# Kernel tuning notes

Measured on AMD Instinct MI355X. Metric: run time of the kernel, lower is better.

Reference implementation:

```python
import jax, jax.numpy as jnp
import numpy as np

NHEAD = 8
DILATED = 1


def setup_inputs() -> dict:
    key = jax.random.key(0)
    ks = jax.random.split(key, 5)
    bs, c, h, w, k = 2, 256, 128, 128, 8
    L = (h // 2) * (w // 2)
    return {
        "query": jax.random.normal(ks[0], (bs, c, h, w), jnp.float32),
        "key": jax.random.normal(ks[1], (bs, c, h, w), jnp.float32),
        "value": jax.random.normal(ks[2], (bs, c, h, w), jnp.float32),
        "topk_pos": jax.random.randint(ks[3], (bs, L, k, 2), 0, h // 2, dtype=jnp.int32).astype(jnp.int64),
        "rel_pos": jax.random.normal(ks[4], (bs, NHEAD, h, w, 4 * k), jnp.float32),
    }


def reference(query, key, value, topk_pos, rel_pos):
    bs, c, h0, w0 = query.shape
    h1, w1 = key.shape[2], key.shape[3]
    nh = NHEAD
    d = c // nh
    L = (h0 // 2) * (w0 // 2)
    k = topk_pos.shape[2]
    k4 = 4 * k

    # key/value: [b,c,h,w] -> [b, h1*w1, nh, d]
    kf = key.reshape(bs, c, h1 * w1).transpose(0, 2, 1).reshape(bs, h1 * w1, nh, d)
    vf = value.reshape(bs, c, h1 * w1).transpose(0, 2, 1).reshape(bs, h1 * w1, nh, d)

    # query grouped into 2x2 blocks: [b, L, 4, nh, d]
    q = query.reshape(bs, nh, d, h0 // 2, 2, w0 // 2, 2)
    q = q.transpose(0, 3, 5, 4, 6, 1, 2).reshape(bs, L, 4, nh, d)

    # build gather indices into flattened key grid (offsets by dilation)
    tp = topk_pos * 2                               # [b, L, k, 2]
    row, col = tp[..., 0], tp[..., 1]
    offs = [(0, 0), (0, DILATED), (DILATED, 0), (DILATED, DILATED)]
    idx = jnp.stack([(row + x) * w1 + (col + y) for x, y in offs], axis=3)  # [b,L,k,4]
    idx = jnp.clip(idx, 0, h1 * w1 - 1).reshape(bs, L, k4)

    def gather(tbl):  # tbl: [b, h1*w1, nh, d] -> [b, L, k4, nh, d]
        return jax.vmap(lambda t, i: t[i])(tbl, idx.reshape(bs, L * k4)).reshape(bs, L, k4, nh, d)

    kg = gather(kf)
    vg = gather(vf)

    scale = 1.0 / np.sqrt(d).astype(np.float32)
    qk = jnp.einsum('blthd,blmhd->bltmh', q, kg) * scale  # [b,L,4,k4,nh]

    rp = rel_pos.reshape(bs, nh, h0 // 2, 2, w0 // 2, 2, k4)
    rp = rp.transpose(0, 2, 4, 3, 5, 6, 1).reshape(bs, L, 4, k4, nh)
    qk = qk + rp

    A = jax.nn.softmax(qk, axis=-2)  # softmax over the k*4 candidate axis
    msg = jnp.einsum('bltmh,blmhd->blthd', A, vg)  # [b,L,4,nh,d]

    # un-group 2x2 blocks back to full resolution: [b, h0*w0, c]
    msg = msg.reshape(bs, h0 // 2, w0 // 2, 2, 2, nh, d)
    msg = msg.transpose(0, 1, 3, 2, 4, 5, 6).reshape(bs, h0 * w0, c)

    up_idx = jnp.broadcast_to(idx[:, :, None, :], (bs, L, 4, k4))
    up_idx = up_idx.reshape(bs, h0 // 2, w0 // 2, 2, 2, k4)
    up_idx = up_idx.transpose(0, 1, 3, 2, 4, 5).reshape(bs, h0 * w0, k4)
    return msg, up_idx
```

## Files before the change

### kernel.cpp

```cpp
#include <hip/hip_runtime.h>
#include <hip/hip_fp16.h>
#include <math.h>

constexpr int NH = 8;
constexpr int D = 32;
constexpr int C = 256;
constexpr int H0 = 128;
constexpr int W0 = 128;
constexpr int PIX = H0 * W0;
constexpr int LBLK = 4096;
constexpr int K4 = 32;
constexpr int KSTH = 260;
constexpr int KST = 258;

__global__ __launch_bounds__(256) void transpose_qkv_kernel(
    const float* __restrict__ q, const float* __restrict__ k,
    const float* __restrict__ v, float* __restrict__ qT,
    __half* __restrict__ kT, __half* __restrict__ vT)
{
  __shared__ float tile[64 * 65];
  const int z = blockIdx.z;
  const int b = z & 1;
  const int arr = z >> 1;
  const float* src = (arr == 0 ? q : arr == 1 ? k : v) + (size_t)b * C * PIX;

  const int p0 = blockIdx.x * 64;
  const int c0 = blockIdx.y * 64;
  const int t15 = threadIdx.x & 15;
  const int thi4 = threadIdx.x >> 4;

#pragma unroll
  for (int r = 0; r < 4; ++r) {
    const int ch = thi4 + r * 16;
    const int p4 = t15 * 4;
    float4 f = *(const float4*)&src[(size_t)(c0 + ch) * PIX + p0 + p4];
    tile[(p4 + 0) * 65 + ch] = f.x;
    tile[(p4 + 1) * 65 + ch] = f.y;
    tile[(p4 + 2) * 65 + ch] = f.z;
    tile[(p4 + 3) * 65 + ch] = f.w;
  }
  __syncthreads();

  if (arr == 0) {
    float* dst = qT + (size_t)b * PIX * C;
#pragma unroll
    for (int r = 0; r < 4; ++r) {
      const int p = thi4 + r * 16;
      const int c4 = t15 * 4;
      const float* tr = &tile[p * 65 + c4];
      *(float4*)&dst[(size_t)(p0 + p) * C + c0 + c4] =
          make_float4(tr[0], tr[1], tr[2], tr[3]);
    }
  } else {
    __half* dst = (arr == 1 ? kT : vT) + (size_t)b * PIX * C;
    const int t7 = threadIdx.x & 7;
    const int th8 = threadIdx.x >> 3;
#pragma unroll
    for (int r = 0; r < 2; ++r) {
      const int p = th8 + r * 32;
      const int c8 = t7 * 8;
      const float* tr = &tile[p * 65 + c8];
      __half2 h0 = __floats2half2_rn(tr[0], tr[1]);
      __half2 h1 = __floats2half2_rn(tr[2], tr[3]);
      __half2 h2 = __floats2half2_rn(tr[4], tr[5]);
      __half2 h3 = __floats2half2_rn(tr[6], tr[7]);
      uint4 u;
      u.x = *(unsigned*)&h0; u.y = *(unsigned*)&h1;
      u.z = *(unsigned*)&h2; u.w = *(unsigned*)&h3;
      *(uint4*)&dst[(size_t)(p0 + p) * C + c0 + c8] = u;
    }
  }
}

__global__ __launch_bounds__(256) void cascade_attn_f16(
    const float* __restrict__ qT,
    const __half* __restrict__ kT,
    const __half* __restrict__ vT,
    const int* __restrict__ topk,
    const float* __restrict__ relp,
    float* __restrict__ out_msg,
    float* __restrict__ out_idx)
{
  __shared__ __half kvh[K4 * KSTH];
  __shared__ float qa[4 * C];

  const int tid = threadIdx.x;
  const int bid = blockIdx.x;
  const int b = bid >> 12;
  const int l = bid & (LBLK - 1);
  const int by = l >> 6, bx = l & 63;
  const int r0 = by * 2, c0 = bx * 2;

  const int* tp = topk + ((size_t)b * LBLK + l) * 16;

  const int h = tid >> 5;
  const int m = tid & 31;

  {
    const int t = tid >> 6, ln = tid & 63;
    const int pix = r0 * W0 + c0 + (t >> 1) * W0 + (t & 1);
    float4 f = *(const float4*)&qT[((size_t)b * PIX + pix) * C + ln * 4];
    *(float4*)&qa[t * C + ln * 4] = f;
  }

  const int p = tid >> 3;
  const int ln8 = tid & 7;
  const int jj = p >> 2, o = p & 3;
  const int gpix = (tp[jj * 2] * 2 + (o >> 1)) * W0 + tp[jj * 2 + 1] * 2 + (o & 1);

  {
    const __half* src = &kT[((size_t)b * PIX + gpix) * C + ln8 * 8];
#pragma unroll
    for (int i = 0; i < 4; ++i) {
      uint4 f = *(const uint4*)(src + i * 64);
      __half* dst = &kvh[p * KSTH + ln8 * 8 + i * 64];
      *(uint2*)dst = make_uint2(f.x, f.y);
      *(uint2*)(dst + 4) = make_uint2(f.z, f.w);
    }
  }

  uint4 vreg[4];
  {
    const __half* src = &vT[((size_t)b * PIX + gpix) * C + ln8 * 8];
#pragma unroll
    for (int i = 0; i < 4; ++i) vreg[i] = *(const uint4*)(src + i * 64);
  }

  const size_t rb = ((((size_t)b * NH + h) * H0 + r0) * W0 + c0) * K4 + m;
  float rl0 = relp[rb];
  float rl1 = relp[rb + K4];
  float rl2 = relp[rb + (size_t)W0 * K4];
  float rl3 = relp[rb + (size_t)W0 * K4 + K4];

  if (tid < 128) {
    const int mm = tid & 31, t = tid >> 5;
    const int j2 = mm >> 2, o2 = mm & 3;
    const int pix = (tp[j2 * 2] * 2 + (o2 >> 1)) * W0 + tp[j2 * 2 + 1] * 2 + (o2 & 1);
    const int prow = r0 + (t >> 1), pcol = c0 + (t & 1);
    out_idx[((size_t)b * PIX + prow * W0 + pcol) * K4 + mm] = (float)pix;
  }
  __syncthreads();

  float a0 = 0.f, a1 = 0.f, a2 = 0.f, a3 = 0.f;
#pragma unroll
  for (int dq = 0; dq < 8; ++dq) {
    const int off = h * D + dq * 4;
    float4 q0 = *(const float4*)&qa[0 * C + off];
    float4 q1 = *(const float4*)&qa[1 * C + off];
    float4 q2 = *(const float4*)&qa[2 * C + off];
    float4 q3 = *(const float4*)&qa[3 * C + off];
    uint2 kraw = *(const uint2*)&kvh[m * KSTH + off];
    __half2 kh0 = *(__half2*)&kraw.x;
    __half2 kh1 = *(__half2*)&kraw.y;
    float2 ka = __half22float2(kh0);
    float2 kc = __half22float2(kh1);
    a0 += q0.x * ka.x + q0.y * ka.y + q0.z * kc.x + q0.w * kc.y;
    a1 += q1.x * ka.x + q1.y * ka.y + q1.z * kc.x + q1.w * kc.y;
    a2 += q2.x * ka.x + q2.y * ka.y + q2.z * kc.x + q2.w * kc.y;
    a3 += q3.x * ka.x + q3.y * ka.y + q3.z * kc.x + q3.w * kc.y;
  }

  const float scale = 0.17677669529663687f;
  float sv[4];
  sv[0] = a0 * scale + rl0;
  sv[1] = a1 * scale + rl1;
  sv[2] = a2 * scale + rl2;
  sv[3] = a3 * scale + rl3;

  float pr4[4];
#pragma unroll
  for (int t = 0; t < 4; ++t) {
    float x = sv[t];
    float mx = x;
#pragma unroll
    for (int off = 16; off > 0; off >>= 1) mx = fmaxf(mx, __shfl_xor(mx, off));
    float pbit = __expf(x - mx);
    float sm = pbit;
#pragma unroll
    for (int off = 16; off > 0; off >>= 1) sm += __shfl_xor(sm, off);
    pr4[t] = pbit / sm;
  }
  __syncthreads();

  *(float4*)&qa[tid * 4] = make_float4(pr4[0], pr4[1], pr4[2], pr4[3]);
#pragma unroll
  for (int i = 0; i < 4; ++i) {
    __half* dst = &kvh[p * KSTH + ln8 * 8 + i * 64];
    *(uint2*)dst = make_uint2(vreg[i].x, vreg[i].y);
    *(uint2*)(dst + 4) = make_uint2(vreg[i].z, vreg[i].w);
  }
  __syncthreads();

  float o0 = 0.f, o1 = 0.f, o2 = 0.f, o3 = 0.f;
#pragma unroll
  for (int mm = 0; mm < 32; ++mm) {
    float4 a4 = *(const float4*)&qa[(h * K4 + mm) * 4];
    float vv = __half2float(kvh[mm * KSTH + h * D + m]);
    o0 += a4.x * vv;
    o1 += a4.y * vv;
    o2 += a4.z * vv;
    o3 += a4.w * vv;
  }
  const size_t ob = ((size_t)b * PIX + (size_t)r0 * W0 + c0) * C + h * D + m;
  out_msg[ob] = o0;
  out_msg[ob + C] = o1;
  out_msg[ob + (size_t)W0 * C] = o2;
  out_msg[ob + (size_t)W0 * C + C] = o3;
}

__global__ __launch_bounds__(256) void cascade_attn_fallback(
    const float* __restrict__ query, const float* __restrict__ key,
    const float* __restrict__ value, const int* __restrict__ topk,
    const float* __restrict__ relp, float* __restrict__ out_msg,
    float* __restrict__ out_idx)
{
  __shared__ float kv[K4 * KST];
  __shared__ float qs[4 * C];
  __shared__ float as_[NH * K4 * 4];

  const int tid = threadIdx.x;
  const int bid = blockIdx.x;
  const int b = bid >> 12;
  const int l = bid & (LBLK - 1);
  const int by = l >> 6, bx = l & 63;
  const int r0 = by * 2, c0 = bx * 2;

  const size_t plane = (size_t)PIX;
  const float* qb = query + (size_t)b * C * plane;
  const float* kb = key + (size_t)b * C * plane;
  const float* vb = value + (size_t)b * C * plane;
  const int* tp = topk + ((size_t)b * LBLK + l) * 16;

  {
    const float* qp = qb + (size_t)tid * plane + r0 * W0 + c0;
    float2 a = *(const float2*)qp;
    float2 bb = *(const float2*)(qp + W0);
    qs[0 * C + tid] = a.x; qs[1 * C + tid] = a.y;
    qs[2 * C + tid] = bb.x; qs[3 * C + tid] = bb.y;
  }
#pragma unroll
  for (int it = 0; it < 16; ++it) {
    const int jj = it >> 1, x = it & 1;
    const int pr = tp[jj * 2] * 2 + x;
    const int pc = tp[jj * 2 + 1] * 2;
    float2 f = *(const float2*)(kb + (size_t)tid * plane + pr * W0 + pc);
    const int m0 = jj * 4 + x * 2;
    kv[m0 * KST + tid] = f.x;
    kv[(m0 + 1) * KST + tid] = f.y;
  }
  if (tid < 128) {
    const int m = tid & 31, t = tid >> 5;
    const int jj = m >> 2, o = m & 3;
    const int pix = (tp[jj * 2] * 2 + (o >> 1)) * W0 + tp[jj * 2 + 1] * 2 + (o & 1);
    const int prow = r0 + (t >> 1), pcol = c0 + (t & 1);
    out_idx[((size_t)b * plane + prow * W0 + pcol) * K4 + m] = (float)pix;
  }
  __syncthreads();

  const int h = tid >> 5;
  const int m = tid & 31;
  float a0 = 0.f, a1 = 0.f, a2 = 0.f, a3 = 0.f;
#pragma unroll
  for (int dq = 0; dq < 8; ++dq) {
    const int off = h * D + dq * 4;
    float4 q0 = *(const float4*)&qs[0 * C + off];
    float4 q1 = *(const float4*)&qs[1 * C + off];
    float4 q2 = *(const float4*)&qs[2 * C + off];
    float4 q3 = *(const float4*)&qs[3 * C + off];
    float2 ka = *(const float2*)&kv[m * KST + off];
    float2 kc = *(const float2*)&kv[m * KST + off + 2];
    a0 += q0.x * ka.x + q0.y * ka.y + q0.z * kc.x + q0.w * kc.y;
    a1 += q1.x * ka.x + q1.y * ka.y + q1.z * kc.x + q1.w * kc.y;
    a2 += q2.x * ka.x + q2.y * ka.y + q2.z * kc.x + q2.w * kc.y;
    a3 += q3.x * ka.x + q3.y * ka.y + q3.z * kc.x + q3.w * kc.y;
  }
  const float scale = 0.17677669529663687f;
  const size_t rb = ((((size_t)b * NH + h) * H0 + r0) * W0 + c0) * K4 + m;
  float sv[4];
  sv[0] = a0 * scale + relp[rb];
  sv[1] = a1 * scale + relp[rb + K4];
  sv[2] = a2 * scale + relp[rb + (size_t)W0 * K4];
  sv[3] = a3 * scale + relp[rb + (size_t)W0 * K4 + K4];
  float pr4[4];
#pragma unroll
  for (int t = 0; t < 4; ++t) {
    float x = sv[t];
    float mx = x;
#pragma unroll
    for (int off = 16; off > 0; off >>= 1) mx = fmaxf(mx, __shfl_xor(mx, off));
    float pbit = __expf(x - mx);
    float sm = pbit;
#pragma unroll
    for (int off = 16; off > 0; off >>= 1) sm += __shfl_xor(sm, off);
    pr4[t] = pbit / sm;
  }
  *(float4*)&as_[tid * 4] = make_float4(pr4[0], pr4[1], pr4[2], pr4[3]);
  __syncthreads();
#pragma unroll
  for (int it = 0; it < 16; ++it) {
    const int jj = it >> 1, x = it & 1;
    const int pr = tp[jj * 2] * 2 + x;
    const int pc = tp[jj * 2 + 1] * 2;
    float2 f = *(const float2*)(vb + (size_t)tid * plane + pr * W0 + pc);
    const int m0 = jj * 4 + x * 2;
    kv[m0 * KST + tid] = f.x;
    kv[(m0 + 1) * KST + tid] = f.y;
  }
  __syncthreads();
  float o0 = 0.f, o1 = 0.f, o2 = 0.f, o3 = 0.f;
#pragma unroll
  for (int mm = 0; mm < 32; ++mm) {
    float4 a4 = *(const float4*)&as_[(h * K4 + mm) * 4];
    float vv = kv[mm * KST + h * D + m];
    o0 += a4.x * vv; o1 += a4.y * vv; o2 += a4.z * vv; o3 += a4.w * vv;
  }
  const size_t ob = ((size_t)b * plane + (size_t)r0 * W0 + c0) * C + h * D + m;
  out_msg[ob] = o0;
  out_msg[ob + C] = o1;
  out_msg[ob + (size_t)W0 * C] = o2;
  out_msg[ob + (size_t)W0 * C + C] = o3;
}

extern "C" void kernel_launch(void* const* d_in, const int* in_sizes, int n_in,
                              void* d_out, int out_size, void* d_ws, size_t ws_size,
                              hipStream_t stream) {
  const float* q = (const float*)d_in[0];
  const float* k = (const float*)d_in[1];
  const float* v = (const float*)d_in[2];
  const int* tp = (const int*)d_in[3];
  const float* rp = (const float*)d_in[4];

  float* out_msg = (float*)d_out;
  float* out_idx = out_msg + (size_t)2 * PIX * C;

  const size_t n_elem = (size_t)2 * PIX * C;
  const size_t needed = n_elem * sizeof(float) + 2 * n_elem * sizeof(__half);
  if (ws_size >= needed) {
    float* qT = (float*)d_ws;
    __half* kT = (__half*)(qT + n_elem);
    __half* vT = kT + n_elem;
    dim3 tg(PIX / 64, C / 64, 6);
    hipLaunchKernelGGL(transpose_qkv_kernel, tg, dim3(256), 0, stream,
                       q, k, v, qT, kT, vT);
    hipLaunchKernelGGL(cascade_attn_f16, dim3(2 * LBLK), dim3(256), 0, stream,
                       qT, kT, vT, tp, rp, out_msg, out_idx);
  } else {
    hipLaunchKernelGGL(cascade_attn_fallback, dim3(2 * LBLK), dim3(256), 0, stream,
                       q, k, v, tp, rp, out_msg, out_idx);
  }
}
```

Before: 208.9 us.

## Drop query transpose, load K into registers, use fdot2 and shuffles

The query is no longer transposed into a float workspace. The attention kernel reads it directly from NCHW with strided float2 loads, converts it to fp16 in shared memory, and the transpose kernel now only handles K and V. Each lane gathers its own key row into registers and computes QK with packed fp16 dot instructions (fdot2). Softmax probabilities are broadcast by warp shuffles instead of through shared memory, which removes two block syncs and the V staging round trip. The costs are uncoalesced strided query reads, lower precision for Q, and many shuffles in the PV loop.

```diff
diff --git a/kernel.cpp b/kernel.cpp
--- a/kernel.cpp
+++ b/kernel.cpp
@@ -13,16 +13,32 @@
 constexpr int KSTH = 260;
 constexpr int KST = 258;
 
-__global__ __launch_bounds__(256) void transpose_qkv_kernel(
-    const float* __restrict__ q, const float* __restrict__ k,
-    const float* __restrict__ v, float* __restrict__ qT,
+typedef _Float16 half2_t __attribute__((ext_vector_type(2)));
+
+#if defined(__has_builtin)
+#if __has_builtin(__builtin_amdgcn_fdot2)
+#define HAVE_FDOT2 1
+#endif
+#endif
+
+__device__ __forceinline__ float fdot2_acc(half2_t a, half2_t b, float c) {
+#ifdef HAVE_FDOT2
+  return __builtin_amdgcn_fdot2(a, b, c, false);
+#else
+  return c + (float)a.x * (float)b.x + (float)a.y * (float)b.y;
+#endif
+}
+
+__global__ __launch_bounds__(256) void transpose_kv_kernel(
+    const float* __restrict__ k, const float* __restrict__ v,
     __half* __restrict__ kT, __half* __restrict__ vT)
 {
   __shared__ float tile[64 * 65];
   const int z = blockIdx.z;
   const int b = z & 1;
   const int arr = z >> 1;
-  const float* src = (arr == 0 ? q : arr == 1 ? k : v) + (size_t)b * C * PIX;
+  const float* src = (arr == 0 ? k : v) + (size_t)b * C * PIX;
+  __half* dst = (arr == 0 ? kT : vT) + (size_t)b * PIX * C;
 
   const int p0 = blockIdx.x * 64;
   const int c0 = blockIdx.y * 64;
@@ -41,39 +57,26 @@
   }
   __syncthreads();
 
-  if (arr == 0) {
-    float* dst = qT + (size_t)b * PIX * C;
-#pragma unroll
-    for (int r = 0; r < 4; ++r) {
-      const int p = thi4 + r * 16;
-      const int c4 = t15 * 4;
-      const float* tr = &tile[p * 65 + c4];
-      *(float4*)&dst[(size_t)(p0 + p) * C + c0 + c4] =
-          make_float4(tr[0], tr[1], tr[2], tr[3]);
-    }
-  } else {
-    __half* dst = (arr == 1 ? kT : vT) + (size_t)b * PIX * C;
-    const int t7 = threadIdx.x & 7;
-    const int th8 = threadIdx.x >> 3;
-#pragma unroll
-    for (int r = 0; r < 2; ++r) {
-      const int p = th8 + r * 32;
-      const int c8 = t7 * 8;
-      const float* tr = &tile[p * 65 + c8];
-      __half2 h0 = __floats2half2_rn(tr[0], tr[1]);
-      __half2 h1 = __floats2half2_rn(tr[2], tr[3]);
-      __half2 h2 = __floats2half2_rn(tr[4], tr[5]);
-      __half2 h3 = __floats2half2_rn(tr[6], tr[7]);
-      uint4 u;
-      u.x = *(unsigned*)&h0; u.y = *(unsigned*)&h1;
-      u.z = *(unsigned*)&h2; u.w = *(unsigned*)&h3;
-      *(uint4*)&dst[(size_t)(p0 + p) * C + c0 + c8] = u;
-    }
+  const int t7 = threadIdx.x & 7;
+  const int th8 = threadIdx.x >> 3;
+#pragma unroll
+  for (int r = 0; r < 2; ++r) {
+    const int p = th8 + r * 32;
+    const int c8 = t7 * 8;
+    const float* tr = &tile[p * 65 + c8];
+    __half2 h0 = __floats2half2_rn(tr[0], tr[1]);
+    __half2 h1 = __floats2half2_rn(tr[2], tr[3]);
+    __half2 h2 = __floats2half2_rn(tr[4], tr[5]);
+    __half2 h3 = __floats2half2_rn(tr[6], tr[7]);
+    uint4 u;
+    u.x = *(unsigned*)&h0; u.y = *(unsigned*)&h1;
+    u.z = *(unsigned*)&h2; u.w = *(unsigned*)&h3;
+    *(uint4*)&dst[(size_t)(p0 + p) * C + c0 + c8] = u;
   }
 }
 
 __global__ __launch_bounds__(256) void cascade_attn_f16(
-    const float* __restrict__ qT,
+    const float* __restrict__ query,
     const __half* __restrict__ kT,
     const __half* __restrict__ vT,
     const int* __restrict__ topk,
@@ -81,8 +84,8 @@
     float* __restrict__ out_msg,
     float* __restrict__ out_idx)
 {
-  __shared__ __half kvh[K4 * KSTH];
-  __shared__ float qa[4 * C];
+  __shared__ __half vsh[K4 * KSTH];
+  __shared__ __half qh[4 * C];
 
   const int tid = threadIdx.x;
   const int bid = blockIdx.x;
@@ -97,33 +100,37 @@
   const int m = tid & 31;
 
   {
-    const int t = tid >> 6, ln = tid & 63;
-    const int pix = r0 * W0 + c0 + (t >> 1) * W0 + (t & 1);
-    float4 f = *(const float4*)&qT[((size_t)b * PIX + pix) * C + ln * 4];
-    *(float4*)&qa[t * C + ln * 4] = f;
+    const float* qp = query + (size_t)b * C * PIX + (size_t)tid * PIX + r0 * W0 + c0;
+    float2 qa = *(const float2*)qp;
+    float2 qb = *(const float2*)(qp + W0);
+    qh[0 * C + tid] = __float2half(qa.x);
+    qh[1 * C + tid] = __float2half(qa.y);
+    qh[2 * C + tid] = __float2half(qb.x);
+    qh[3 * C + tid] = __float2half(qb.y);
   }
 
   const int p = tid >> 3;
   const int ln8 = tid & 7;
-  const int jj = p >> 2, o = p & 3;
-  const int gpix = (tp[jj * 2] * 2 + (o >> 1)) * W0 + tp[jj * 2 + 1] * 2 + (o & 1);
-
   {
-    const __half* src = &kT[((size_t)b * PIX + gpix) * C + ln8 * 8];
+    const int jj = p >> 2, o = p & 3;
+    const int gp = (tp[jj * 2] * 2 + (o >> 1)) * W0 + tp[jj * 2 + 1] * 2 + (o & 1);
+    const __half* src = &vT[((size_t)b * PIX + gp) * C + ln8 * 8];
 #pragma unroll
     for (int i = 0; i < 4; ++i) {
       uint4 f = *(const uint4*)(src + i * 64);
-      __half* dst = &kvh[p * KSTH + ln8 * 8 + i * 64];
+      __half* dst = &vsh[p * KSTH + ln8 * 8 + i * 64];
       *(uint2*)dst = make_uint2(f.x, f.y);
       *(uint2*)(dst + 4) = make_uint2(f.z, f.w);
     }
   }
 
-  uint4 vreg[4];
+  uint4 kr[4];
   {
-    const __half* src = &vT[((size_t)b * PIX + gpix) * C + ln8 * 8];
-#pragma unroll
-    for (int i = 0; i < 4; ++i) vreg[i] = *(const uint4*)(src + i * 64);
+    const int jj = m >> 2, o = m & 3;
+    const int gp = (tp[jj * 2] * 2 + (o >> 1)) * W0 + tp[jj * 2 + 1] * 2 + (o & 1);
+    const __half* src = &kT[((size_t)b * PIX + gp) * C + h * D];
+#pragma unroll
+    for (int i = 0; i < 4; ++i) kr[i] = *(const uint4*)(src + i * 8);
   }
 
   const size_t rb = ((((size_t)b * NH + h) * H0 + r0) * W0 + c0) * K4 + m;
@@ -141,31 +148,21 @@
   }
   __syncthreads();
 
-  float a0 = 0.f, a1 = 0.f, a2 = 0.f, a3 = 0.f;
-#pragma unroll
-  for (int dq = 0; dq < 8; ++dq) {
-    const int off = h * D + dq * 4;
-    float4 q0 = *(const float4*)&qa[0 * C + off];
-    float4 q1 = *(const float4*)&qa[1 * C + off];
-    float4 q2 = *(const float4*)&qa[2 * C + off];
-    float4 q3 = *(const float4*)&qa[3 * C + off];
-    uint2 kraw = *(const uint2*)&kvh[m * KSTH + off];
-    __half2 kh0 = *(__half2*)&kraw.x;
-    __half2 kh1 = *(__half2*)&kraw.y;
-    float2 ka = __half22float2(kh0);
-    float2 kc = __half22float2(kh1);
-    a0 += q0.x * ka.x + q0.y * ka.y + q0.z * kc.x + q0.w * kc.y;
-    a1 += q1.x * ka.x + q1.y * ka.y + q1.z * kc.x + q1.w * kc.y;
-    a2 += q2.x * ka.x + q2.y * ka.y + q2.z * kc.x + q2.w * kc.y;
-    a3 += q3.x * ka.x + q3.y * ka.y + q3.z * kc.x + q3.w * kc.y;
+  const half2_t* kh = (const half2_t*)kr;
+  float acc[4] = {0.f, 0.f, 0.f, 0.f};
+#pragma unroll
+  for (int t = 0; t < 4; ++t) {
+    const half2_t* qrow = (const half2_t*)&qh[t * C + h * D];
+#pragma unroll
+    for (int i = 0; i < 16; ++i) acc[t] = fdot2_acc(qrow[i], kh[i], acc[t]);
   }
 
   const float scale = 0.17677669529663687f;
   float sv[4];
-  sv[0] = a0 * scale + rl0;
-  sv[1] = a1 * scale + rl1;
-  sv[2] = a2 * scale + rl2;
-  sv[3] = a3 * scale + rl3;
+  sv[0] = acc[0] * scale + rl0;
+  sv[1] = acc[1] * scale + rl1;
+  sv[2] = acc[2] * scale + rl2;
+  sv[3] = acc[3] * scale + rl3;
 
   float pr4[4];
 #pragma unroll
@@ -180,26 +177,17 @@
     for (int off = 16; off > 0; off >>= 1) sm += __shfl_xor(sm, off);
     pr4[t] = pbit / sm;
   }
-  __syncthreads();
-
-  *(float4*)&qa[tid * 4] = make_float4(pr4[0], pr4[1], pr4[2], pr4[3]);
-#pragma unroll
-  for (int i = 0; i < 4; ++i) {
-    __half* dst = &kvh[p * KSTH + ln8 * 8 + i * 64];
-    *(uint2*)dst = make_uint2(vreg[i].x, vreg[i].y);
-    *(uint2*)(dst + 4) = make_uint2(vreg[i].z, vreg[i].w);
-  }
-  __syncthreads();
-
+
+  const int lanebase = tid & 32;
   float o0 = 0.f, o1 = 0.f, o2 = 0.f, o3 = 0.f;
 #pragma unroll
   for (int mm = 0; mm < 32; ++mm) {
-    float4 a4 = *(const float4*)&qa[(h * K4 + mm) * 4];
-    float vv = __half2float(kvh[mm * KSTH + h * D + m]);
-    o0 += a4.x * vv;
-    o1 += a4.y * vv;
-    o2 += a4.z * vv;
-    o3 += a4.w * vv;
+    float vv = __half2float(vsh[mm * KSTH + h * D + m]);
+    const int src = lanebase + mm;
+    o0 += __shfl(pr4[0], src) * vv;
+    o1 += __shfl(pr4[1], src) * vv;
+    o2 += __shfl(pr4[2], src) * vv;
+    o3 += __shfl(pr4[3], src) * vv;
   }
   const size_t ob = ((size_t)b * PIX + (size_t)r0 * W0 + c0) * C + h * D + m;
   out_msg[ob] = o0;
@@ -334,16 +322,14 @@
   float* out_idx = out_msg + (size_t)2 * PIX * C;
 
   const size_t n_elem = (size_t)2 * PIX * C;
-  const size_t needed = n_elem * sizeof(float) + 2 * n_elem * sizeof(__half);
+  const size_t needed = 2 * n_elem * sizeof(__half);
   if (ws_size >= needed) {
-    float* qT = (float*)d_ws;
-    __half* kT = (__half*)(qT + n_elem);
+    __half* kT = (__half*)d_ws;
     __half* vT = kT + n_elem;
-    dim3 tg(PIX / 64, C / 64, 6);
-    hipLaunchKernelGGL(transpose_qkv_kernel, tg, dim3(256), 0, stream,
-                       q, k, v, qT, kT, vT);
+    dim3 tg(PIX / 64, C / 64, 4);
+    hipLaunchKernelGGL(transpose_kv_kernel, tg, dim3(256), 0, stream, k, v, kT, vT);
     hipLaunchKernelGGL(cascade_attn_f16, dim3(2 * LBLK), dim3(256), 0, stream,
-                       qT, kT, vT, tp, rp, out_msg, out_idx);
+                       q, kT, vT, tp, rp, out_msg, out_idx);
   } else {
     hipLaunchKernelGGL(cascade_attn_fallback, dim3(2 * LBLK), dim3(256), 0, stream,
                        q, k, v, tp, rp, out_msg, out_idx);
```

Measured after the change: 225.8 us. +8.1%, slower.
